# Optimization experiments

Measured on AMD Instinct MI355X. Metric: run time of the kernel, lower is better.

## Reference

```python
import jax, jax.numpy as jnp
import numpy as np

N = 8192      # number of patches (nodes)
DIN = 384     # input feature dim
DH = 512      # hidden dim
K = 6         # topk neighbors
NC = 2        # n_classes


def setup_inputs() -> dict:
    key = jax.random.key(0)
    ks = jax.random.split(key, 20)
    def w(k, shape):
        fan_in = shape[0]
        return jax.random.normal(k, shape, dtype=jnp.float32) * (1.0 / np.sqrt(fan_in))
    return {
        "x_s":   jax.random.normal(ks[0], (N, DIN), dtype=jnp.float32),
        "fc1_w": w(ks[1], (DIN, DH)), "fc1_b": jnp.zeros((DH,), jnp.float32),
        "wh_w":  w(ks[2], (DH, DH)),  "wh_b":  jnp.zeros((DH,), jnp.float32),
        "wt_w":  w(ks[3], (DH, DH)),  "wt_b":  jnp.zeros((DH,), jnp.float32),
        "l1_w":  w(ks[4], (DH, DH)),  "l1_b":  jnp.zeros((DH,), jnp.float32),
        "l2_w":  w(ks[5], (DH, DH)),  "l2_b":  jnp.zeros((DH,), jnp.float32),
        "att1_w": w(ks[6], (DH, DH // 2)), "att1_b": jnp.zeros((DH // 2,), jnp.float32),
        "att2_w": w(ks[7], (DH // 2, 1)),  "att2_b": jnp.zeros((1,), jnp.float32),
        "ln_g":  jnp.ones((DH,), jnp.float32), "ln_b": jnp.zeros((DH,), jnp.float32),
        "fc_w":  w(ks[8], (DH, NC)), "fc_b": jnp.zeros((NC,), jnp.float32),
    }


def reference(x_s, fc1_w, fc1_b, wh_w, wh_b, wt_w, wt_b,
              l1_w, l1_b, l2_w, l2_b, att1_w, att1_b, att2_w, att2_b,
              ln_g, ln_b, fc_w, fc_b):
    lrelu = jax.nn.leaky_relu  # negative_slope=0.01, torch default
    # _fc1 + mean-centering mix (batch dim of 1 dropped; mean is over nodes)
    x = lrelu(x_s @ fc1_w + fc1_b)                       # [N, DH]
    x = (x + x.mean(axis=0, keepdims=True)) * 0.5
    e_h = x @ wh_w + wh_b                                # [N, DH]
    e_t = x @ wt_w + wt_b                                # [N, DH]
    scale = DH ** -0.5
    attn_logit = (e_h * scale) @ e_t.T                   # [N, N] dense scores
    topk_w, topk_i = jax.lax.top_k(attn_logit, K)        # [N, K]
    Nb_h = e_t[topk_i]                                   # gather neighbors [N, K, DH]
    p = jax.nn.softmax(topk_w, axis=1)[..., None]        # [N, K, 1]
    eh_r = p * Nb_h + (1.0 - p) * e_h[:, None, :]        # outer-product form == broadcast
    gate = jnp.tanh(e_h[:, None, :] + eh_r)              # [N, K, DH]
    ka = jnp.einsum('nkd,nkd->nk', Nb_h, gate)           # [N, K]
    ka_p = jax.nn.softmax(ka, axis=1)
    e_Nh = jnp.einsum('nk,nkd->nd', ka_p, Nb_h)          # [N, DH]
    # bi-interaction aggregation (dropout = identity in eval)
    emb = lrelu((e_h + e_Nh) @ l1_w + l1_b) + lrelu((e_h * e_Nh) @ l2_w + l2_b)
    # global attention readout over nodes
    a = lrelu(emb @ att1_w + att1_b) @ att2_w + att2_b   # [N, 1]
    g = jax.nn.softmax(a, axis=0)
    h = (g * emb).sum(axis=0, keepdims=True)             # [1, DH]
    # layernorm (eps=1e-5)
    mu = h.mean(axis=-1, keepdims=True)
    var = ((h - mu) ** 2).mean(axis=-1, keepdims=True)
    hn = (h - mu) / jnp.sqrt(var + 1e-5) * ln_g + ln_b
    logits = hn @ fc_w + fc_b                            # [1, NC]
    return logits
```

## Files before the change

### kernel.cpp

```cpp
#include <hip/hip_runtime.h>
#include <hip/hip_bf16.h>
#include <math.h>

#define N_NODES 8192
#define DIN 384
#define DH 512
#define KNB 6
#define NEG_SLOPE 0.01f
#define NSPLIT 4

typedef __attribute__((ext_vector_type(8))) short bf16x8;
typedef __attribute__((ext_vector_type(4))) float f32x4;

__device__ __forceinline__ unsigned short f2bf(float x) {
  unsigned int u = __float_as_uint(x);
  unsigned int r = (u + 0x7fffu + ((u >> 16) & 1u)) >> 16;
  return (unsigned short)r;
}
__device__ __forceinline__ float bf2f(unsigned short u) {
  return __uint_as_float(((unsigned int)u) << 16);
}

__global__ __launch_bounds__(256) void prep_weights(
    const float* __restrict__ w0, const float* __restrict__ w1,
    const float* __restrict__ w2, const float* __restrict__ w3,
    const float* __restrict__ w4, const float* __restrict__ w5,
    unsigned short* __restrict__ pool) {
  const int f = blockIdx.x * 256 + threadIdx.x;
  const int E0 = 196608, E1 = 458752, E2 = 720896, E3 = 983040, E4 = 1245184, E5 = 1376256;
  if (f >= E5) return;
  const float* src; int off, Kw, Nw;
  if (f < E0)      { src = w0; off = 0;  Kw = 384; Nw = 512; }
  else if (f < E1) { src = w1; off = E0; Kw = 512; Nw = 512; }
  else if (f < E2) { src = w2; off = E1; Kw = 512; Nw = 512; }
  else if (f < E3) { src = w3; off = E2; Kw = 512; Nw = 512; }
  else if (f < E4) { src = w4; off = E3; Kw = 512; Nw = 512; }
  else             { src = w5; off = E4; Kw = 512; Nw = 256; }
  const int local = f - off;
  const int n = local / Kw, k = local - n * Kw;
  pool[f] = f2bf(src[(size_t)k * Nw + n]);
}

__global__ __launch_bounds__(256) void convert_xs(const float* __restrict__ xs,
                                                  unsigned short* __restrict__ out) {
  const size_t i = ((size_t)blockIdx.x * 256 + threadIdx.x) * 4;
  const float4 v = *reinterpret_cast<const float4*>(xs + i);
  ushort4 o;
  o.x = f2bf(v.x); o.y = f2bf(v.y); o.z = f2bf(v.z); o.w = f2bf(v.w);
  *reinterpret_cast<ushort4*>(out + i) = o;
}

template <int ACT, int WF32, int WBF16>
__global__ __launch_bounds__(256) void gemm128(
    const unsigned short* __restrict__ A, const unsigned short* __restrict__ Wt,
    const float* __restrict__ bias, float* __restrict__ C,
    unsigned short* __restrict__ Cb, int K, int N) {
  __shared__ unsigned short sa[128 * 64];
  __shared__ unsigned short sb[128 * 64];
  const int tid = threadIdx.x;
  const int wave = tid >> 6, lane = tid & 63;
  const int lo16 = lane & 15, hi = lane >> 4;
  const int wr = (wave >> 1) << 6, wc = (wave & 1) << 6;
  const int row0 = blockIdx.y << 7, col0 = blockIdx.x << 7;
  f32x4 acc[4][4];
#pragma unroll
  for (int rt = 0; rt < 4; ++rt)
#pragma unroll
    for (int ct = 0; ct < 4; ++ct) { acc[rt][ct].x = 0.f; acc[rt][ct].y = 0.f; acc[rt][ct].z = 0.f; acc[rt][ct].w = 0.f; }
  for (int k0 = 0; k0 < K; k0 += 64) {
    __syncthreads();
#pragma unroll
    for (int i = 0; i < 4; ++i) {
      const int c = i * 256 + tid;
      const int r = c >> 3, i8 = c & 7;
      const bf16x8 va = *reinterpret_cast<const bf16x8*>(A + (size_t)(row0 + r) * K + k0 + i8 * 8);
      const bf16x8 vb = *reinterpret_cast<const bf16x8*>(Wt + (size_t)(col0 + r) * K + k0 + i8 * 8);
      const int byte = r * 128 + ((i8 * 16) ^ ((r & 7) << 4));
      *reinterpret_cast<bf16x8*>(reinterpret_cast<char*>(sa) + byte) = va;
      *reinterpret_cast<bf16x8*>(reinterpret_cast<char*>(sb) + byte) = vb;
    }
    __syncthreads();
#pragma unroll
    for (int kk2 = 0; kk2 < 2; ++kk2) {
      const int inner = (kk2 << 6) + (hi << 4);
      bf16x8 af[4], bf[4];
#pragma unroll
      for (int t = 0; t < 4; ++t) {
        const int row = wr + t * 16 + lo16;
        af[t] = *reinterpret_cast<const bf16x8*>(reinterpret_cast<const char*>(sa) + row * 128 + (inner ^ ((row & 7) << 4)));
        const int col = wc + t * 16 + lo16;
        bf[t] = *reinterpret_cast<const bf16x8*>(reinterpret_cast<const char*>(sb) + col * 128 + (inner ^ ((col & 7) << 4)));
      }
#pragma unroll
      for (int rt = 0; rt < 4; ++rt)
#pragma unroll
        for (int ct = 0; ct < 4; ++ct)
          acc[rt][ct] = __builtin_amdgcn_mfma_f32_16x16x32_bf16(af[rt], bf[ct], acc[rt][ct], 0, 0, 0);
    }
  }
#pragma unroll
  for (int ct = 0; ct < 4; ++ct) {
    const int colg = col0 + wc + ct * 16 + lo16;
    const float bv = bias[colg];
#pragma unroll
    for (int rt = 0; rt < 4; ++rt) {
#pragma unroll
      for (int j = 0; j < 4; ++j) {
        const int r = row0 + wr + rt * 16 + hi * 4 + j;
        float v = acc[rt][ct][j] + bv;
        if (ACT) v = v > 0.f ? v : NEG_SLOPE * v;
        if (WF32) C[(size_t)r * N + colg] = v;
        if (WBF16) Cb[(size_t)r * N + colg] = f2bf(v);
      }
    }
  }
}

__global__ __launch_bounds__(256) void gemm128_ehet(
    const unsigned short* __restrict__ A,
    const unsigned short* __restrict__ W1, const unsigned short* __restrict__ W2,
    const float* __restrict__ b1, const float* __restrict__ b2,
    float* __restrict__ C1, unsigned short* __restrict__ EHb,
    float* __restrict__ C2, unsigned short* __restrict__ ETp, float kscale) {
  __shared__ unsigned short sa[128 * 64];
  __shared__ unsigned short sb1[128 * 64];
  __shared__ unsigned short sb2[128 * 64];
  const int tid = threadIdx.x;
  const int wave = tid >> 6, lane = tid & 63;
  const int lo16 = lane & 15, hi = lane >> 4;
  const int wr = (wave >> 1) << 6, wc = (wave & 1) << 6;
  const int row0 = blockIdx.y << 7, col0 = blockIdx.x << 7;
  f32x4 au[4][4], av[4][4];
#pragma unroll
  for (int rt = 0; rt < 4; ++rt)
#pragma unroll
    for (int ct = 0; ct < 4; ++ct) {
      au[rt][ct].x = 0.f; au[rt][ct].y = 0.f; au[rt][ct].z = 0.f; au[rt][ct].w = 0.f;
      av[rt][ct].x = 0.f; av[rt][ct].y = 0.f; av[rt][ct].z = 0.f; av[rt][ct].w = 0.f;
    }
  for (int k0 = 0; k0 < DH; k0 += 64) {
    __syncthreads();
#pragma unroll
    for (int i = 0; i < 4; ++i) {
      const int c = i * 256 + tid;
      const int r = c >> 3, i8 = c & 7;
      const int byte = r * 128 + ((i8 * 16) ^ ((r & 7) << 4));
      *reinterpret_cast<bf16x8*>(reinterpret_cast<char*>(sa) + byte) =
          *reinterpret_cast<const bf16x8*>(A + (size_t)(row0 + r) * DH + k0 + i8 * 8);
      *reinterpret_cast<bf16x8*>(reinterpret_cast<char*>(sb1) + byte) =
          *reinterpret_cast<const bf16x8*>(W1 + (size_t)(col0 + r) * DH + k0 + i8 * 8);
      *reinterpret_cast<bf16x8*>(reinterpret_cast<char*>(sb2) + byte) =
          *reinterpret_cast<const bf16x8*>(W2 + (size_t)(col0 + r) * DH + k0 + i8 * 8);
    }
    __syncthreads();
#pragma unroll
    for (int kk2 = 0; kk2 < 2; ++kk2) {
      const int inner = (kk2 << 6) + (hi << 4);
      bf16x8 af[4], bf1[4], bf2[4];
#pragma unroll
      for (int t = 0; t < 4; ++t) {
        const int row = wr + t * 16 + lo16;
        const int aoff = row * 128 + (inner ^ ((row & 7) << 4));
        af[t] = *reinterpret_cast<const bf16x8*>(reinterpret_cast<const char*>(sa) + aoff);
        const int col = wc + t * 16 + lo16;
        const int boff = col * 128 + (inner ^ ((col & 7) << 4));
        bf1[t] = *reinterpret_cast<const bf16x8*>(reinterpret_cast<const char*>(sb1) + boff);
        bf2[t] = *reinterpret_cast<const bf16x8*>(reinterpret_cast<const char*>(sb2) + boff);
      }
#pragma unroll
      for (int rt = 0; rt < 4; ++rt)
#pragma unroll
        for (int ct = 0; ct < 4; ++ct) {
          au[rt][ct] = __builtin_amdgcn_mfma_f32_16x16x32_bf16(af[rt], bf1[ct], au[rt][ct], 0, 0, 0);
          av[rt][ct] = __builtin_amdgcn_mfma_f32_16x16x32_bf16(af[rt], bf2[ct], av[rt][ct], 0, 0, 0);
        }
    }
  }
#pragma unroll
  for (int ct = 0; ct < 4; ++ct) {
    const int colg = col0 + wc + ct * 16 + lo16;
    const float bv1 = b1[colg], bv2 = b2[colg];
#pragma unroll
    for (int rt = 0; rt < 4; ++rt) {
#pragma unroll
      for (int j = 0; j < 4; ++j) {
        const int r = row0 + wr + rt * 16 + hi * 4 + j;
        const float vh = au[rt][ct][j] + bv1;
        const float vt = av[rt][ct][j] + bv2;
        C1[(size_t)r * DH + colg] = vh;
        EHb[(size_t)r * DH + colg] = f2bf(vh * kscale);
        C2[(size_t)r * DH + colg] = vt;
        const size_t idx = (size_t)(r >> 4) * 8192 + (size_t)(colg >> 5) * 512 +
                           (size_t)((((colg & 31) >> 3) * 16 + (r & 15)) * 8) + (colg & 7);
        ETp[idx] = f2bf(vt);
      }
    }
  }
}

__global__ __launch_bounds__(256) void gemm128_l1l2(
    const unsigned short* __restrict__ Ub, const unsigned short* __restrict__ Vb,
    const unsigned short* __restrict__ W1, const unsigned short* __restrict__ W2,
    const float* __restrict__ b1, const float* __restrict__ b2,
    unsigned short* __restrict__ EMBb) {
  __shared__ unsigned short sa1[128 * 64];
  __shared__ unsigned short sa2[128 * 64];
  __shared__ unsigned short sb1[128 * 64];
  __shared__ unsigned short sb2[128 * 64];
  const int tid = threadIdx.x;
  const int wave = tid >> 6, lane = tid & 63;
  const int lo16 = lane & 15, hi = lane >> 4;
  const int wr = (wave >> 1) << 6, wc = (wave & 1) << 6;
  const int row0 = blockIdx.y << 7, col0 = blockIdx.x << 7;
  f32x4 au[4][4], av[4][4];
#pragma unroll
  for (int rt = 0; rt < 4; ++rt)
#pragma unroll
    for (int ct = 0; ct < 4; ++ct) {
      au[rt][ct].x = 0.f; au[rt][ct].y = 0.f; au[rt][ct].z = 0.f; au[rt][ct].w = 0.f;
      av[rt][ct].x = 0.f; av[rt][ct].y = 0.f; av[rt][ct].z = 0.f; av[rt][ct].w = 0.f;
    }
  for (int k0 = 0; k0 < DH; k0 += 64) {
    __syncthreads();
#pragma unroll
    for (int i = 0; i < 4; ++i) {
      const int c = i * 256 + tid;
      const int r = c >> 3, i8 = c & 7;
      const int byte = r * 128 + ((i8 * 16) ^ ((r & 7) << 4));
      *reinterpret_cast<bf16x8*>(reinterpret_cast<char*>(sa1) + byte) =
          *reinterpret_cast<const bf16x8*>(Ub + (size_t)(row0 + r) * DH + k0 + i8 * 8);
      *reinterpret_cast<bf16x8*>(reinterpret_cast<char*>(sa2) + byte) =
          *reinterpret_cast<const bf16x8*>(Vb + (size_t)(row0 + r) * DH + k0 + i8 * 8);
      *reinterpret_cast<bf16x8*>(reinterpret_cast<char*>(sb1) + byte) =
          *reinterpret_cast<const bf16x8*>(W1 + (size_t)(col0 + r) * DH + k0 + i8 * 8);
      *reinterpret_cast<bf16x8*>(reinterpret_cast<char*>(sb2) + byte) =
          *reinterpret_cast<const bf16x8*>(W2 + (size_t)(col0 + r) * DH + k0 + i8 * 8);
    }
    __syncthreads();
#pragma unroll
    for (int kk2 = 0; kk2 < 2; ++kk2) {
      const int inner = (kk2 << 6) + (hi << 4);
      bf16x8 a1[4], a2[4], bf1[4], bf2[4];
#pragma unroll
      for (int t = 0; t < 4; ++t) {
        const int row = wr + t * 16 + lo16;
        const int aoff = row * 128 + (inner ^ ((row & 7) << 4));
        a1[t] = *reinterpret_cast<const bf16x8*>(reinterpret_cast<const char*>(sa1) + aoff);
        a2[t] = *reinterpret_cast<const bf16x8*>(reinterpret_cast<const char*>(sa2) + aoff);
        const int col = wc + t * 16 + lo16;
        const int boff = col * 128 + (inner ^ ((col & 7) << 4));
        bf1[t] = *reinterpret_cast<const bf16x8*>(reinterpret_cast<const char*>(sb1) + boff);
        bf2[t] = *reinterpret_cast<const bf16x8*>(reinterpret_cast<const char*>(sb2) + boff);
      }
#pragma unroll
      for (int rt = 0; rt < 4; ++rt)
#pragma unroll
        for (int ct = 0; ct < 4; ++ct) {
          au[rt][ct] = __builtin_amdgcn_mfma_f32_16x16x32_bf16(a1[rt], bf1[ct], au[rt][ct], 0, 0, 0);
          av[rt][ct] = __builtin_amdgcn_mfma_f32_16x16x32_bf16(a2[rt], bf2[ct], av[rt][ct], 0, 0, 0);
        }
    }
  }
#pragma unroll
  for (int ct = 0; ct < 4; ++ct) {
    const int colg = col0 + wc + ct * 16 + lo16;
    const float bv1 = b1[colg], bv2 = b2[colg];
#pragma unroll
    for (int rt = 0; rt < 4; ++rt) {
#pragma unroll
      for (int j = 0; j < 4; ++j) {
        const int r = row0 + wr + rt * 16 + hi * 4 + j;
        float u = au[rt][ct][j] + bv1;
        float v = av[rt][ct][j] + bv2;
        u = u > 0.f ? u : NEG_SLOPE * u;
        v = v > 0.f ? v : NEG_SLOPE * v;
        EMBb[(size_t)r * DH + colg] = f2bf(u + v);
      }
    }
  }
}

__global__ __launch_bounds__(256) void colsum_kernel(const float* __restrict__ X,
                                                     float* __restrict__ cs) {
  const int tid = threadIdx.x;
  float s0 = 0.f, s1 = 0.f;
  const int r0 = blockIdx.x * 128;
  for (int r = r0; r < r0 + 128; ++r) {
    s0 += X[(size_t)r * DH + tid];
    s1 += X[(size_t)r * DH + tid + 256];
  }
  atomicAdd(&cs[tid], s0);
  atomicAdd(&cs[tid + 256], s1);
}

__global__ __launch_bounds__(256) void mix_kernel(float* __restrict__ X,
                                                  const float* __restrict__ cs,
                                                  unsigned short* __restrict__ Xb) {
  const size_t gid = (size_t)blockIdx.x * 256 + threadIdx.x;
  const int c4 = ((int)gid & 127) << 2;
  float4 x = *reinterpret_cast<float4*>(X + gid * 4);
  const float inv = 1.f / 8192.f;
  x.x = (x.x + cs[c4 + 0] * inv) * 0.5f;
  x.y = (x.y + cs[c4 + 1] * inv) * 0.5f;
  x.z = (x.z + cs[c4 + 2] * inv) * 0.5f;
  x.w = (x.w + cs[c4 + 3] * inv) * 0.5f;
  ushort4 o;
  o.x = f2bf(x.x); o.y = f2bf(x.y); o.z = f2bf(x.z); o.w = f2bf(x.w);
  *reinterpret_cast<ushort4*>(Xb + gid * 4) = o;
}

__global__ __launch_bounds__(512, 2) void score_topk_v3(
    const unsigned short* __restrict__ EHb, const unsigned short* __restrict__ ETp,
    float* __restrict__ tkv, int* __restrict__ tki) {
  __shared__ unsigned short sa[128 * 512];
  __shared__ float swb[8][8 * 68];
  const int tid = threadIdx.x;
  const int wave = tid >> 6, lane = tid & 63;
  const int lo16 = lane & 15, hi = lane >> 4;
  const int bid = blockIdx.x;
  const int split = (bid & 7) >> 1;
  const int rowblk = ((bid >> 3) << 1) | (bid & 1);
  const int grow0 = rowblk << 7;
  const int colbase0 = split << 11;

#pragma unroll
  for (int i = 0; i < 16; ++i) {
    const int c = i * 512 + tid;
    const int row = c >> 6, i8 = c & 63;
    const bf16x8 v = *reinterpret_cast<const bf16x8*>(
        EHb + (size_t)(grow0 + row) * DH + i8 * 8);
    const int byte = row * 1024 + ((i8 * 16) ^ ((row & 7) << 4));
    *reinterpret_cast<bf16x8*>(reinterpret_cast<char*>(sa) + byte) = v;
  }
  __syncthreads();

  float tv[2][6];
  int ti[2][6];
#pragma unroll
  for (int a = 0; a < 2; ++a)
#pragma unroll
    for (int s = 0; s < 6; ++s) { tv[a][s] = -3.4e38f; ti[a][s] = 0; }

  float* sw = swb[wave];

  bf16x8 bcur[4];
  {
    const int jg0 = (colbase0 + wave * 64) >> 4;
#pragma unroll
    for (int ct = 0; ct < 4; ++ct)
      bcur[ct] = *reinterpret_cast<const bf16x8*>(
          ETp + (size_t)(jg0 + ct) * 8192 + lane * 8);
  }

  for (int jt = 0; jt < 4; ++jt) {
    const int wcol0 = colbase0 + jt * 512 + wave * 64;
    const int jgbase = wcol0 >> 4;
    f32x4 acc[8][4];
#pragma unroll
    for (int rt = 0; rt < 8; ++rt)
#pragma unroll
      for (int ct = 0; ct < 4; ++ct) {
        acc[rt][ct].x = 0.f; acc[rt][ct].y = 0.f; acc[rt][ct].z = 0.f; acc[rt][ct].w = 0.f;
      }
#pragma unroll
    for (int kk = 0; kk < 16; ++kk) {
      bf16x8 bnxt[4];
      if (kk < 15) {
#pragma unroll
        for (int ct = 0; ct < 4; ++ct)
          bnxt[ct] = *reinterpret_cast<const bf16x8*>(
              ETp + (size_t)(jgbase + ct) * 8192 + (kk + 1) * 512 + lane * 8);
      } else {
        const int jtn = (jt == 3) ? 3 : (jt + 1);
        const int jgn = (colbase0 + jtn * 512 + wave * 64) >> 4;
#pragma unroll
        for (int ct = 0; ct < 4; ++ct)
          bnxt[ct] = *reinterpret_cast<const bf16x8*>(
              ETp + (size_t)(jgn + ct) * 8192 + lane * 8);
      }
      const int inner = (kk << 6) + (hi << 4);
#pragma unroll
      for (int rt = 0; rt < 8; ++rt) {
        const int row = rt * 16 + lo16;
        const bf16x8 af = *reinterpret_cast<const bf16x8*>(
            reinterpret_cast<const char*>(sa) + row * 1024 + (inner ^ ((row & 7) << 4)));
#pragma unroll
        for (int ct = 0; ct < 4; ++ct)
          acc[rt][ct] = __builtin_amdgcn_mfma_f32_16x16x32_bf16(af, bcur[ct], acc[rt][ct], 0, 0, 0);
      }
#pragma unroll
      for (int ct = 0; ct < 4; ++ct) bcur[ct] = bnxt[ct];
    }
#pragma unroll
    for (int a = 0; a < 2; ++a) {
#pragma unroll
      for (int ct = 0; ct < 4; ++ct) {
#pragma unroll
        for (int h = 0; h < 2; ++h) {
          if ((lo16 >> 3) == h) {
#pragma unroll
            for (int rtl = 0; rtl < 4; ++rtl)
              *reinterpret_cast<f32x4*>(sw + (lo16 & 7) * 68 + rtl * 16 + hi * 4) =
                  acc[a * 4 + rtl][ct];
          }
          asm volatile("s_waitcnt lgkmcnt(0)" ::: "memory");
#pragma unroll
          for (int cc = 0; cc < 8; ++cc) {
            const float v = sw[cc * 68 + lane];
            const int col = wcol0 + ct * 16 + h * 8 + cc;
            if (v > tv[a][5]) {
              tv[a][5] = v; ti[a][5] = col;
#pragma unroll
              for (int p = 5; p > 0; --p) {
                if (tv[a][p] > tv[a][p - 1]) {
                  float tvt = tv[a][p]; tv[a][p] = tv[a][p - 1]; tv[a][p - 1] = tvt;
                  int tit = ti[a][p]; ti[a][p] = ti[a][p - 1]; ti[a][p - 1] = tit;
                }
              }
            }
          }
          asm volatile("s_waitcnt lgkmcnt(0)" ::: "memory");
        }
      }
    }
  }
  __syncthreads();
  float* mv = reinterpret_cast<float*>(sa);
  int* mi = reinterpret_cast<int*>(mv + 128 * 8 * 6);
#pragma unroll
  for (int a = 0; a < 2; ++a) {
    const int row = a * 64 + lane;
#pragma unroll
    for (int s = 0; s < 6; ++s) {
      mv[(row * 8 + wave) * 6 + s] = tv[a][s];
      mi[(row * 8 + wave) * 6 + s] = ti[a][s];
    }
  }
  __syncthreads();
  if (tid < 128) {
    int pq[8] = {0, 0, 0, 0, 0, 0, 0, 0};
    const int base = (split * N_NODES + grow0 + tid) * 6;
    for (int s = 0; s < 6; ++s) {
      float best = -3.4e38f;
      int bi = 0x7fffffff, bq = 0;
#pragma unroll
      for (int q = 0; q < 8; ++q) {
        if (pq[q] < 6) {
          const float v = mv[(tid * 8 + q) * 6 + pq[q]];
          const int ix = mi[(tid * 8 + q) * 6 + pq[q]];
          if (v > best || (v == best && ix < bi)) { best = v; bi = ix; bq = q; }
        }
      }
      tkv[base + s] = best;
      tki[base + s] = bi;
#pragma unroll
      for (int q = 0; q < 8; ++q) pq[q] += (bq == q) ? 1 : 0;
    }
  }
}

__global__ __launch_bounds__(256) void merge_topk4(const float* __restrict__ tkv,
                                                   const int* __restrict__ tki,
                                                   float* __restrict__ fw,
                                                   int* __restrict__ fi) {
  const int n = blockIdx.x * 256 + threadIdx.x;
  int pq[NSPLIT] = {0, 0, 0, 0};
  for (int s = 0; s < 6; ++s) {
    float best = -3.4e38f;
    int bi = 0x7fffffff, bq = 0;
#pragma unroll
    for (int q = 0; q < NSPLIT; ++q) {
      if (pq[q] < 6) {
        const float v = tkv[((size_t)q * N_NODES + n) * 6 + pq[q]];
        const int ix = tki[((size_t)q * N_NODES + n) * 6 + pq[q]];
        if (v > best || (v == best && ix < bi)) { best = v; bi = ix; bq = q; }
      }
    }
    fw[n * 6 + s] = best;
    fi[n * 6 + s] = bi;
#pragma unroll
    for (int q = 0; q < NSPLIT; ++q) pq[q] += (bq == q) ? 1 : 0;
  }
}

__global__ __launch_bounds__(256) void agg_kernel(const float* __restrict__ EH,
                                                  const float* __restrict__ ET,
                                                  const float* __restrict__ fw,
                                                  const int* __restrict__ fi,
                                                  unsigned short* __restrict__ Ub,
                                                  unsigned short* __restrict__ Vb) {
  __shared__ float sNb[KNB][DH];
  __shared__ float sred[4][8];
  __shared__ float ska[8];
  const int node = blockIdx.x;
  const int tid = threadIdx.x;
  float w[KNB];
  int idx[KNB];
#pragma unroll
  for (int k = 0; k < KNB; ++k) {
    w[k] = fw[node * KNB + k];
    idx[k] = fi[node * KNB + k];
  }
  float mx = w[0];
#pragma unroll
  for (int k = 1; k < KNB; ++k) mx = fmaxf(mx, w[k]);
  float pk[KNB];
  float se = 0.f;
#pragma unroll
  for (int k = 0; k < KNB; ++k) { pk[k] = expf(w[k] - mx); se += pk[k]; }
  const float inv_se = 1.f / se;
#pragma unroll
  for (int k = 0; k < KNB; ++k) pk[k] *= inv_se;
  for (int e = tid; e < KNB * DH; e += 256) {
    int k = e >> 9, d = e & 511;
    sNb[k][d] = ET[(size_t)idx[k] * DH + d];
  }
  __syncthreads();
  float eh[2];
  eh[0] = EH[(size_t)node * DH + tid];
  eh[1] = EH[(size_t)node * DH + tid + 256];
  float ka[KNB] = {0, 0, 0, 0, 0, 0};
#pragma unroll
  for (int t = 0; t < 2; ++t) {
    const int d = tid + t * 256;
    const float e_ = eh[t];
#pragma unroll
    for (int k = 0; k < KNB; ++k) {
      float Nb = sNb[k][d];
      float ehr = pk[k] * Nb + (1.f - pk[k]) * e_;
      float g = tanhf(e_ + ehr);
      ka[k] = fmaf(Nb, g, ka[k]);
    }
  }
#pragma unroll
  for (int k = 0; k < KNB; ++k) {
    float v = ka[k];
#pragma unroll
    for (int off = 32; off > 0; off >>= 1) v += __shfl_down(v, off, 64);
    if ((tid & 63) == 0) sred[tid >> 6][k] = v;
  }
  __syncthreads();
  if (tid < KNB) ska[tid] = sred[0][tid] + sred[1][tid] + sred[2][tid] + sred[3][tid];
  __syncthreads();
  float kav[KNB];
#pragma unroll
  for (int k = 0; k < KNB; ++k) kav[k] = ska[k];
  float kmx = kav[0];
#pragma unroll
  for (int k = 1; k < KNB; ++k) kmx = fmaxf(kmx, kav[k]);
  float kp[KNB];
  float ks = 0.f;
#pragma unroll
  for (int k = 0; k < KNB; ++k) { kp[k] = expf(kav[k] - kmx); ks += kp[k]; }
  const float inv_ks = 1.f / ks;
#pragma unroll
  for (int k = 0; k < KNB; ++k) kp[k] *= inv_ks;
#pragma unroll
  for (int t = 0; t < 2; ++t) {
    const int d = tid + t * 256;
    float eNh = 0.f;
#pragma unroll
    for (int k = 0; k < KNB; ++k) eNh = fmaf(kp[k], sNb[k][d], eNh);
    const float e_ = eh[t];
    Ub[(size_t)node * DH + d] = f2bf(e_ + eNh);
    Vb[(size_t)node * DH + d] = f2bf(e_ * eNh);
  }
}

__global__ __launch_bounds__(256) void att_dot(const unsigned short* __restrict__ HIDb,
                                               const float* __restrict__ w2,
                                               const float* __restrict__ b2,
                                               float* __restrict__ a) {
  const int wid = threadIdx.x >> 6, lane = threadIdx.x & 63;
  const int node = blockIdx.x * 4 + wid;
  const ushort4 h4 = *reinterpret_cast<const ushort4*>(HIDb + (size_t)node * 256 + lane * 4);
  const float4 w4 = *reinterpret_cast<const float4*>(w2 + lane * 4);
  float s = bf2f(h4.x) * w4.x + bf2f(h4.y) * w4.y + bf2f(h4.z) * w4.z + bf2f(h4.w) * w4.w;
#pragma unroll
  for (int off = 32; off > 0; off >>= 1) s += __shfl_down(s, off, 64);
  if (lane == 0) a[node] = s + b2[0];
}

__global__ __launch_bounds__(1024) void softmax_stats(const float* __restrict__ a,
                                                      float* __restrict__ st) {
  __shared__ float red[16];
  __shared__ float bc;
  const int tid = threadIdx.x;
  float mx = -3.4e38f;
  for (int i = tid; i < N_NODES; i += 1024) mx = fmaxf(mx, a[i]);
#pragma unroll
  for (int off = 32; off > 0; off >>= 1) mx = fmaxf(mx, __shfl_xor(mx, off, 64));
  if ((tid & 63) == 0) red[tid >> 6] = mx;
  __syncthreads();
  if (tid == 0) {
    float m = red[0];
    for (int i = 1; i < 16; ++i) m = fmaxf(m, red[i]);
    bc = m;
  }
  __syncthreads();
  const float gm = bc;
  float se = 0.f;
  for (int i = tid; i < N_NODES; i += 1024) se += expf(a[i] - gm);
#pragma unroll
  for (int off = 32; off > 0; off >>= 1) se += __shfl_xor(se, off, 64);
  if ((tid & 63) == 0) red[tid >> 6] = se;
  __syncthreads();
  if (tid == 0) {
    float s = 0.f;
    for (int i = 0; i < 16; ++i) s += red[i];
    st[0] = gm;
    st[1] = s;
  }
}

__global__ __launch_bounds__(256) void readout(const unsigned short* __restrict__ EMBb,
                                               const float* __restrict__ a,
                                               const float* __restrict__ st,
                                               float* __restrict__ h) {
  __shared__ float sacc[4][64];
  const int tid = threadIdx.x;
  const int c = (blockIdx.x << 6) + (tid & 63);
  const int rsub = tid >> 6;
  const float mx = st[0], inv_se = 1.f / st[1];
  const int r0 = blockIdx.y << 8;
  float acc = 0.f;
  for (int i = 0; i < 64; ++i) {
    const int r = r0 + (i << 2) + rsub;
    const float g = expf(a[r] - mx);
    acc = fmaf(g, bf2f(EMBb[(size_t)r * DH + c]), acc);
  }
  sacc[rsub][tid & 63] = acc * inv_se;
  __syncthreads();
  if (rsub == 0) {
    float t = sacc[0][tid] + sacc[1][tid] + sacc[2][tid] + sacc[3][tid];
    atomicAdd(&h[c], t);
  }
}

__global__ __launch_bounds__(512) void finalize(const float* __restrict__ h,
                                                const float* __restrict__ ln_g,
                                                const float* __restrict__ ln_b,
                                                const float* __restrict__ fc_w,
                                                const float* __restrict__ fc_b,
                                                float* __restrict__ out) {
  __shared__ float red0[8];
  __shared__ float red1[8];
  __shared__ float bc[2];
  const int tid = threadIdx.x;
  const int wid = tid >> 6, lane = tid & 63;
  const float v = h[tid];
  float s = v;
#pragma unroll
  for (int off = 32; off > 0; off >>= 1) s += __shfl_xor(s, off, 64);
  if (lane == 0) red0[wid] = s;
  __syncthreads();
  if (tid == 0) {
    float t = 0.f;
    for (int i = 0; i < 8; ++i) t += red0[i];
    bc[0] = t * (1.f / 512.f);
  }
  __syncthreads();
  const float mu = bc[0];
  const float dv = v - mu;
  s = dv * dv;
#pragma unroll
  for (int off = 32; off > 0; off >>= 1) s += __shfl_xor(s, off, 64);
  if (lane == 0) red0[wid] = s;
  __syncthreads();
  if (tid == 0) {
    float t = 0.f;
    for (int i = 0; i < 8; ++i) t += red0[i];
    bc[1] = t * (1.f / 512.f);
  }
  __syncthreads();
  const float var = bc[1];
  const float hn = dv / sqrtf(var + 1e-5f) * ln_g[tid] + ln_b[tid];
  float l0 = hn * fc_w[tid * 2 + 0];
  float l1 = hn * fc_w[tid * 2 + 1];
#pragma unroll
  for (int off = 32; off > 0; off >>= 1) {
    l0 += __shfl_xor(l0, off, 64);
    l1 += __shfl_xor(l1, off, 64);
  }
  if (lane == 0) { red0[wid] = l0; red1[wid] = l1; }
  __syncthreads();
  if (tid == 0) {
    float t0 = 0.f, t1 = 0.f;
    for (int i = 0; i < 8; ++i) { t0 += red0[i]; t1 += red1[i]; }
    out[0] = t0 + fc_b[0];
    out[1] = t1 + fc_b[1];
  }
}

extern "C" void kernel_launch(void* const* d_in, const int* in_sizes, int n_in,
                              void* d_out, int out_size, void* d_ws, size_t ws_size,
                              hipStream_t stream) {
  const float* x_s    = (const float*)d_in[0];
  const float* fc1_w  = (const float*)d_in[1];
  const float* fc1_b  = (const float*)d_in[2];
  const float* wh_w   = (const float*)d_in[3];
  const float* wh_b   = (const float*)d_in[4];
  const float* wt_w   = (const float*)d_in[5];
  const float* wt_b   = (const float*)d_in[6];
  const float* l1_w   = (const float*)d_in[7];
  const float* l1_b   = (const float*)d_in[8];
  const float* l2_w   = (const float*)d_in[9];
  const float* l2_b   = (const float*)d_in[10];
  const float* att1_w = (const float*)d_in[11];
  const float* att1_b = (const float*)d_in[12];
  const float* att2_w = (const float*)d_in[13];
  const float* att2_b = (const float*)d_in[14];
  const float* ln_g   = (const float*)d_in[15];
  const float* ln_b   = (const float*)d_in[16];
  const float* fc_w   = (const float*)d_in[17];
  const float* fc_b   = (const float*)d_in[18];

  float* ws = (float*)d_ws;
  const size_t BIG = (size_t)N_NODES * DH;
  float* B1 = ws;
  float* B2 = ws + BIG;
  unsigned short* R1 = (unsigned short*)(ws + 2 * BIG);
  unsigned short* R2 = R1 + BIG;
  unsigned short* R3 = R2 + BIG;
  unsigned short* WT = R3 + BIG;
  float* tail = (float*)(WT + 1376256);
  float* tkv    = tail;
  int*   tki    = (int*)(tkv + NSPLIT * N_NODES * 6);
  float* fwv    = (float*)(tki + NSPLIT * N_NODES * 6);
  int*   fiv    = (int*)(fwv + N_NODES * 6);
  float* colsum = (float*)(fiv + N_NODES * 6);
  float* av     = colsum + DH;
  float* stats  = av + N_NODES;
  float* hbuf   = stats + 16;

  unsigned short* fc1t  = WT + 0;
  unsigned short* wht   = WT + 196608;
  unsigned short* wtt   = WT + 458752;
  unsigned short* l1t   = WT + 720896;
  unsigned short* l2t   = WT + 983040;
  unsigned short* att1t = WT + 1245184;

  const float kscale = 0.044194173824159216f;

  prep_weights<<<5376, 256, 0, stream>>>(fc1_w, wh_w, wt_w, l1_w, l2_w, att1_w, WT);
  convert_xs<<<3072, 256, 0, stream>>>(x_s, R1);
  gemm128<1, 1, 0><<<dim3(4, 64), 256, 0, stream>>>(
      R1, fc1t, fc1_b, B1, nullptr, DIN, DH);
  hipMemsetAsync(colsum, 0, DH * sizeof(float), stream);
  colsum_kernel<<<64, 256, 0, stream>>>(B1, colsum);
  mix_kernel<<<4096, 256, 0, stream>>>(B1, colsum, R2);
  gemm128_ehet<<<dim3(4, 64), 256, 0, stream>>>(
      R2, wht, wtt, wh_b, wt_b, B1, R1, B2, R3, kscale);
  score_topk_v3<<<256, 512, 0, stream>>>(R1, R3, tkv, tki);
  merge_topk4<<<32, 256, 0, stream>>>(tkv, tki, fwv, fiv);
  agg_kernel<<<N_NODES, 256, 0, stream>>>(B1, B2, fwv, fiv, R1, R2);
  gemm128_l1l2<<<dim3(4, 64), 256, 0, stream>>>(
      R1, R2, l1t, l2t, l1_b, l2_b, R3);
  gemm128<1, 0, 1><<<dim3(2, 64), 256, 0, stream>>>(
      R3, att1t, att1_b, nullptr, R1, DH, 256);
  att_dot<<<2048, 256, 0, stream>>>(R1, att2_w, att2_b, av);
  softmax_stats<<<1, 1024, 0, stream>>>(av, stats);
  hipMemsetAsync(hbuf, 0, DH * sizeof(float), stream);
  readout<<<dim3(8, 32), 256, 0, stream>>>(R3, av, stats, hbuf);
  finalize<<<1, 512, 0, stream>>>(hbuf, ln_g, ln_b, fc_w, fc_b, (float*)d_out);
}
```

Baseline: 406.5 us.

## Shrink score/top-k tiles to 32 rows with 4 waves and split-lane top-k scan

The fused score+top-k kernel now handles 32 query rows per block with 256 threads, launching 1024 blocks instead of 256 blocks of 512 threads with 128 rows. Each lane now scans only 4 of every 8 columns, with two lanes per row keeping separate top-6 lists, and the per-block merge combines eight lists per row. The goal is more parallelism and occupancy, a less serialized top-k scan, and lower LDS and register use. The cost is that each ETp B-fragment loaded from global memory now feeds only 2 row tiles of MFMAs instead of 8, so reuse drops and global/L2 traffic for the key matrix rises about fourfold.

```diff
diff --git a/kernel.cpp b/kernel.cpp
--- a/kernel.cpp
+++ b/kernel.cpp
@@ -309,23 +309,23 @@
   *reinterpret_cast<ushort4*>(Xb + gid * 4) = o;
 }
 
-__global__ __launch_bounds__(512, 2) void score_topk_v3(
+__global__ __launch_bounds__(256, 4) void score_topk_v6(
     const unsigned short* __restrict__ EHb, const unsigned short* __restrict__ ETp,
     float* __restrict__ tkv, int* __restrict__ tki) {
-  __shared__ unsigned short sa[128 * 512];
-  __shared__ float swb[8][8 * 68];
+  __shared__ unsigned short sa[32 * 512];
+  __shared__ float swb[4][8 * 36];
   const int tid = threadIdx.x;
   const int wave = tid >> 6, lane = tid & 63;
   const int lo16 = lane & 15, hi = lane >> 4;
   const int bid = blockIdx.x;
   const int split = (bid & 7) >> 1;
   const int rowblk = ((bid >> 3) << 1) | (bid & 1);
-  const int grow0 = rowblk << 7;
+  const int grow0 = rowblk << 5;
   const int colbase0 = split << 11;
 
 #pragma unroll
-  for (int i = 0; i < 16; ++i) {
-    const int c = i * 512 + tid;
+  for (int i = 0; i < 8; ++i) {
+    const int c = i * 256 + tid;
     const int row = c >> 6, i8 = c & 63;
     const bf16x8 v = *reinterpret_cast<const bf16x8*>(
         EHb + (size_t)(grow0 + row) * DH + i8 * 8);
@@ -334,14 +334,13 @@
   }
   __syncthreads();
 
-  float tv[2][6];
-  int ti[2][6];
-#pragma unroll
-  for (int a = 0; a < 2; ++a)
-#pragma unroll
-    for (int s = 0; s < 6; ++s) { tv[a][s] = -3.4e38f; ti[a][s] = 0; }
+  float tv[6];
+  int ti[6];
+#pragma unroll
+  for (int s = 0; s < 6; ++s) { tv[s] = -3.4e38f; ti[s] = 0; }
 
   float* sw = swb[wave];
+  const int scanr = lane & 31, scang = lane >> 5;
 
   bf16x8 bcur[4];
   {
@@ -352,12 +351,12 @@
           ETp + (size_t)(jg0 + ct) * 8192 + lane * 8);
   }
 
-  for (int jt = 0; jt < 4; ++jt) {
-    const int wcol0 = colbase0 + jt * 512 + wave * 64;
+  for (int jt = 0; jt < 8; ++jt) {
+    const int wcol0 = colbase0 + jt * 256 + wave * 64;
     const int jgbase = wcol0 >> 4;
-    f32x4 acc[8][4];
-#pragma unroll
-    for (int rt = 0; rt < 8; ++rt)
+    f32x4 acc[2][4];
+#pragma unroll
+    for (int rt = 0; rt < 2; ++rt)
 #pragma unroll
       for (int ct = 0; ct < 4; ++ct) {
         acc[rt][ct].x = 0.f; acc[rt][ct].y = 0.f; acc[rt][ct].z = 0.f; acc[rt][ct].w = 0.f;
@@ -371,8 +370,8 @@
           bnxt[ct] = *reinterpret_cast<const bf16x8*>(
               ETp + (size_t)(jgbase + ct) * 8192 + (kk + 1) * 512 + lane * 8);
       } else {
-        const int jtn = (jt == 3) ? 3 : (jt + 1);
-        const int jgn = (colbase0 + jtn * 512 + wave * 64) >> 4;
+        const int jtn = (jt == 7) ? 7 : (jt + 1);
+        const int jgn = (colbase0 + jtn * 256 + wave * 64) >> 4;
 #pragma unroll
         for (int ct = 0; ct < 4; ++ct)
           bnxt[ct] = *reinterpret_cast<const bf16x8*>(
@@ -380,7 +379,7 @@
       }
       const int inner = (kk << 6) + (hi << 4);
 #pragma unroll
-      for (int rt = 0; rt < 8; ++rt) {
+      for (int rt = 0; rt < 2; ++rt) {
         const int row = rt * 16 + lo16;
         const bf16x8 af = *reinterpret_cast<const bf16x8*>(
             reinterpret_cast<const char*>(sa) + row * 1024 + (inner ^ ((row & 7) << 4)));
@@ -392,52 +391,47 @@
       for (int ct = 0; ct < 4; ++ct) bcur[ct] = bnxt[ct];
     }
 #pragma unroll
-    for (int a = 0; a < 2; ++a) {
-#pragma unroll
-      for (int ct = 0; ct < 4; ++ct) {
-#pragma unroll
-        for (int h = 0; h < 2; ++h) {
-          if ((lo16 >> 3) == h) {
-#pragma unroll
-            for (int rtl = 0; rtl < 4; ++rtl)
-              *reinterpret_cast<f32x4*>(sw + (lo16 & 7) * 68 + rtl * 16 + hi * 4) =
-                  acc[a * 4 + rtl][ct];
-          }
-          asm volatile("s_waitcnt lgkmcnt(0)" ::: "memory");
-#pragma unroll
-          for (int cc = 0; cc < 8; ++cc) {
-            const float v = sw[cc * 68 + lane];
-            const int col = wcol0 + ct * 16 + h * 8 + cc;
-            if (v > tv[a][5]) {
-              tv[a][5] = v; ti[a][5] = col;
-#pragma unroll
-              for (int p = 5; p > 0; --p) {
-                if (tv[a][p] > tv[a][p - 1]) {
-                  float tvt = tv[a][p]; tv[a][p] = tv[a][p - 1]; tv[a][p - 1] = tvt;
-                  int tit = ti[a][p]; ti[a][p] = ti[a][p - 1]; ti[a][p - 1] = tit;
-                }
+    for (int ct = 0; ct < 4; ++ct) {
+#pragma unroll
+      for (int h = 0; h < 2; ++h) {
+        if ((lo16 >> 3) == h) {
+#pragma unroll
+          for (int rt = 0; rt < 2; ++rt)
+            *reinterpret_cast<f32x4*>(sw + (lo16 & 7) * 36 + rt * 16 + hi * 4) = acc[rt][ct];
+        }
+        asm volatile("s_waitcnt lgkmcnt(0)" ::: "memory");
+#pragma unroll
+        for (int cc = 0; cc < 4; ++cc) {
+          const float v = sw[(scang * 4 + cc) * 36 + scanr];
+          const int col = wcol0 + ct * 16 + h * 8 + scang * 4 + cc;
+          if (v > tv[5]) {
+            tv[5] = v; ti[5] = col;
+#pragma unroll
+            for (int p = 5; p > 0; --p) {
+              if (tv[p] > tv[p - 1]) {
+                float tvt = tv[p]; tv[p] = tv[p - 1]; tv[p - 1] = tvt;
+                int tit = ti[p]; ti[p] = ti[p - 1]; ti[p - 1] = tit;
               }
             }
           }
-          asm volatile("s_waitcnt lgkmcnt(0)" ::: "memory");
         }
+        asm volatile("s_waitcnt lgkmcnt(0)" ::: "memory");
       }
     }
   }
   __syncthreads();
   float* mv = reinterpret_cast<float*>(sa);
-  int* mi = reinterpret_cast<int*>(mv + 128 * 8 * 6);
-#pragma unroll
-  for (int a = 0; a < 2; ++a) {
-    const int row = a * 64 + lane;
+  int* mi = reinterpret_cast<int*>(mv + 32 * 8 * 6);
+  {
+    const int li = wave * 2 + scang;
 #pragma unroll
     for (int s = 0; s < 6; ++s) {
-      mv[(row * 8 + wave) * 6 + s] = tv[a][s];
-      mi[(row * 8 + wave) * 6 + s] = ti[a][s];
-    }
-  }
-  __syncthreads();
-  if (tid < 128) {
+      mv[(scanr * 8 + li) * 6 + s] = tv[s];
+      mi[(scanr * 8 + li) * 6 + s] = ti[s];
+    }
+  }
+  __syncthreads();
+  if (tid < 32) {
     int pq[8] = {0, 0, 0, 0, 0, 0, 0, 0};
     const int base = (split * N_NODES + grow0 + tid) * 6;
     for (int s = 0; s < 6; ++s) {
@@ -751,7 +745,7 @@
   mix_kernel<<<4096, 256, 0, stream>>>(B1, colsum, R2);
   gemm128_ehet<<<dim3(4, 64), 256, 0, stream>>>(
       R2, wht, wtt, wh_b, wt_b, B1, R1, B2, R3, kscale);
-  score_topk_v3<<<256, 512, 0, stream>>>(R1, R3, tkv, tki);
+  score_topk_v6<<<1024, 256, 0, stream>>>(R1, R3, tkv, tki);
   merge_topk4<<<32, 256, 0, stream>>>(tkv, tki, fwv, fiv);
   agg_kernel<<<N_NODES, 256, 0, stream>>>(B1, B2, fwv, fiv, R1, R2);
   gemm128_l1l2<<<dim3(4, 64), 256, 0, stream>>>(
```

Measured after the change: 357.1 us. -12.1%, faster.
